# Kernel tuning notes

Hardware: AMD Instinct MI355X
Metric: run time of the kernel (lower is better)

The kernel has to match this reference:

```python
import jax, jax.numpy as jnp
import numpy as np

DIM = 2048
NUM_EXPERTS = 64
K = 2
TEMPERATURE = 1.0


def setup_inputs() -> dict:
    key = jax.random.key(0)
    kx, kw, kb = jax.random.split(key, 3)
    x = jax.random.normal(kx, (4, 4096, DIM), dtype=jnp.float32)
    # nn.Linear(dim, num_experts): weight [num_experts, dim], bias [num_experts]
    bound = 1.0 / np.sqrt(DIM)
    W = jax.random.uniform(kw, (NUM_EXPERTS, DIM), dtype=jnp.float32, minval=-bound, maxval=bound)
    b = jax.random.uniform(kb, (NUM_EXPERTS,), dtype=jnp.float32, minval=-bound, maxval=bound)
    return {"x": x, "W": W, "b": b}


def reference(x, W, b):
    # logits: (batch, seq, num_experts)
    logits = (jnp.einsum('bsd,ed->bse', x, W) + b) / TEMPERATURE
    probs = jax.nn.softmax(logits, axis=-1)
    values, indices = jax.lax.top_k(probs, K)
    return indices, values
```

## Files before the change

### kernel.cpp

```cpp
#include <hip/hip_runtime.h>
#include <math.h>

typedef _Float16 half8 __attribute__((ext_vector_type(8)));
typedef float f32x16 __attribute__((ext_vector_type(16)));

#define DIMK 2048
#define NEXP 64
#define BM 32
#define NW 4
#define KPW (DIMK / NW)
#define CHUNK 32
#define NCHUNK (KPW / CHUNK)
#define KSTEP 16
#define NKS (CHUNK / KSTEP)
#define NU (KPW / KSTEP)

__global__ void SwitchRouter_wsplit(const float* __restrict__ W, _Float16* __restrict__ ws) {
    int t = blockIdx.x * 256 + threadIdx.x;
    if (t >= NEXP * DIMK) return;
    int e = t >> 11, k = t & (DIMK - 1);
    float w = W[e * DIMK + k];
    _Float16 h0 = (_Float16)w;
    _Float16 h1 = (_Float16)(w - (float)h0);
    int kb8 = k >> 3, kj = k & 7;
    ws[(((kb8 * 2 + 0) << 9) + (e << 3) + kj)] = h0;
    ws[(((kb8 * 2 + 1) << 9) + (e << 3) + kj)] = h1;
}

__device__ __forceinline__ bool gt_pair(float v, int i, float v2, int i2) {
    return (v > v2) || (v == v2 && i < i2);
}

__device__ __forceinline__ half8 ldw(const _Float16* wsp, int kglob0, int half_, int et, int limb, int row) {
    int kb8 = (kglob0 >> 3) + half_;
    return *(const half8*)(wsp + (((size_t)(kb8 * 2 + limb) << 9) + (((et << 5) + row) << 3)));
}

__global__ __launch_bounds__(256, 3)
void SwitchRouter_43078521979510_kernel(const float* __restrict__ x,
                                        const _Float16* __restrict__ wsp,
                                        const float* __restrict__ bias,
                                        float* __restrict__ out, int M)
{
    __shared__ float lds[8704];

    const int t     = threadIdx.x;
    const int wv    = t >> 6;
    const int lane  = t & 63;
    const int row   = lane & 31;
    const int half_ = lane >> 5;
    const int r0    = blockIdx.x * BM;
    const int kwb   = wv * KPW;

    float* atile = lds + wv * 2048;
    const float* xg0 = x + (size_t)r0 * DIMK + kwb;

#define STAGE(c)                                                                   \
    {                                                                              \
        float* dst = atile + ((c) & 1) * 1024;                                     \
        _Pragma("unroll") for (int j = 0; j < 4; ++j) {                            \
            const int rowj = j * 8 + (lane >> 3);                                  \
            const float* src = xg0 + (size_t)rowj * DIMK + (c) * CHUNK             \
                               + (((lane & 7) ^ (rowj & 7)) << 2);                 \
            __builtin_amdgcn_global_load_lds(                                      \
                (const __attribute__((address_space(1))) void*)src,                \
                (__attribute__((address_space(3))) void*)(dst + j * 256),          \
                16, 0, 0);                                                         \
        }                                                                          \
    }

#define LOADW(u, slot)                                                             \
    {                                                                              \
        const int kg = kwb + (u) * KSTEP;                                          \
        wr[slot][0] = ldw(wsp, kg, half_, 0, 0, row);                              \
        wr[slot][1] = ldw(wsp, kg, half_, 0, 1, row);                              \
        wr[slot][2] = ldw(wsp, kg, half_, 1, 0, row);                              \
        wr[slot][3] = ldw(wsp, kg, half_, 1, 1, row);                              \
    }

    half8 wr[4][4];
    f32x16 acc[2] = {};

    LOADW(0, 0);
    LOADW(1, 1);
    LOADW(2, 2);
    STAGE(0);
    STAGE(1);

    for (int cb = 0; cb < NCHUNK / 2; ++cb) {
#pragma unroll
        for (int pc = 0; pc < 2; ++pc) {
            const int c = 2 * cb + pc;
            if (cb == NCHUNK / 2 - 1 && pc == 1) {
                asm volatile("s_waitcnt vmcnt(0)" ::: "memory");
            } else {
                asm volatile("s_waitcnt vmcnt(4)" ::: "memory");
            }

            const float* buf = atile + pc * 1024;

            float4 fA[NKS], fB[NKS];
#pragma unroll
            for (int ks = 0; ks < NKS; ++ks) {
                const int g  = ks * 4 + half_ * 2;
                const int s0 = g ^ (row & 7);
                const int s1 = (g + 1) ^ (row & 7);
                fA[ks] = *(const float4*)&buf[row * 32 + s0 * 4];
                fB[ks] = *(const float4*)&buf[row * 32 + s1 * 4];
            }
            asm volatile("s_waitcnt lgkmcnt(0)" ::: "memory");
            if (c + 2 < NCHUNK) STAGE(c + 2);

#pragma unroll
            for (int ks = 0; ks < NKS; ++ks) {
                const int u = c * NKS + ks;
                const int slot = (2 * pc + ks) & 3;
                if (u + 3 < NU) LOADW(u + 3, (slot + 3) & 3);

                const float4 va = fA[ks], vb = fB[ks];
                const float f[8] = {va.x, va.y, va.z, va.w, vb.x, vb.y, vb.z, vb.w};
                half8 a0, a1;
#pragma unroll
                for (int j = 0; j < 8; ++j) {
                    _Float16 h = (_Float16)f[j];
                    a0[j] = h;
                    a1[j] = (_Float16)(f[j] - (float)h);
                }

                const half8* w = wr[slot];
                acc[0] = __builtin_amdgcn_mfma_f32_32x32x16_f16(a0, w[0], acc[0], 0, 0, 0);
                acc[0] = __builtin_amdgcn_mfma_f32_32x32x16_f16(a1, w[0], acc[0], 0, 0, 0);
                acc[0] = __builtin_amdgcn_mfma_f32_32x32x16_f16(a0, w[1], acc[0], 0, 0, 0);
                acc[1] = __builtin_amdgcn_mfma_f32_32x32x16_f16(a0, w[2], acc[1], 0, 0, 0);
                acc[1] = __builtin_amdgcn_mfma_f32_32x32x16_f16(a1, w[2], acc[1], 0, 0, 0);
                acc[1] = __builtin_amdgcn_mfma_f32_32x32x16_f16(a0, w[3], acc[1], 0, 0, 0);
            }
        }
    }

    __syncthreads();
    float* red = lds;
#pragma unroll
    for (int s = 0; s < 16; ++s) {
        const int rowD = (s & 3) + 8 * (s >> 2) + 4 * half_;
        red[wv * 2176 + rowD * 68 + 0 * 32 + row] = acc[0][s];
        red[wv * 2176 + rowD * 68 + 1 * 32 + row] = acc[1][s];
    }
    __syncthreads();

    {
        const int rr = t >> 3;
        const int g8 = t & 7;
        float l[8];
#pragma unroll
        for (int j = 0; j < 8; ++j) {
            float s = 0.f;
#pragma unroll
            for (int w2 = 0; w2 < NW; ++w2) s += red[w2 * 2176 + rr * 68 + g8 * 8 + j];
            l[j] = s + bias[g8 * 8 + j];
        }

        float v0 = l[0];
        int   i0 = 8 * g8;
        float v1 = -INFINITY;
        int   i1 = -1;
#pragma unroll
        for (int j = 1; j < 8; ++j) {
            const float lv = l[j];
            const int   e  = 8 * g8 + j;
            if (lv > v0) { v1 = v0; i1 = i0; v0 = lv; i0 = e; }
            else if (lv > v1) { v1 = lv; i1 = e; }
        }
#pragma unroll
        for (int m2 = 1; m2 <= 4; m2 <<= 1) {
            const float ov0 = __shfl_xor(v0, m2);
            const int   oi0 = __shfl_xor(i0, m2);
            const float ov1 = __shfl_xor(v1, m2);
            const int   oi1 = __shfl_xor(i1, m2);
            if (gt_pair(ov0, oi0, v0, i0)) {
                if (gt_pair(v0, i0, ov1, oi1)) { v1 = v0; i1 = i0; }
                else                           { v1 = ov1; i1 = oi1; }
                v0 = ov0; i0 = oi0;
            } else if (gt_pair(ov0, oi0, v1, i1)) {
                v1 = ov0; i1 = oi0;
            }
        }
        float d = 0.f;
#pragma unroll
        for (int j = 0; j < 8; ++j) d += expf(l[j] - v0);
#pragma unroll
        for (int m2 = 1; m2 <= 4; m2 <<= 1) d += __shfl_xor(d, m2);

        if (g8 == 0) {
            const int R = r0 + rr;
            out[2 * R]     = (float)i0;
            out[2 * R + 1] = (float)i1;
            out[2 * M + 2 * R]     = 1.f / d;
            out[2 * M + 2 * R + 1] = expf(v1 - v0) / d;
        }
    }
}

extern "C" void kernel_launch(void* const* d_in, const int* in_sizes, int n_in,
                              void* d_out, int out_size, void* d_ws, size_t ws_size,
                              hipStream_t stream) {
    const float* x  = (const float*)d_in[0];
    const float* W  = (const float*)d_in[1];
    const float* b  = (const float*)d_in[2];
    float* out = (float*)d_out;
    _Float16* ws = (_Float16*)d_ws;
    const int M = in_sizes[0] / DIMK;

    SwitchRouter_wsplit<<<(NEXP * DIMK + 255) / 256, 256, 0, stream>>>(W, ws);
    SwitchRouter_43078521979510_kernel<<<M / BM, 256, 0, stream>>>(x, ws, b, out, M);
}
```

Measured before the change: 34.13 us.

## Fuse weight fp16 split into main kernel, drop separate preprocessing launch

Removes the separate kernel that split W into hi/lo fp16 limbs in a workspace. The main kernel now loads fp32 W directly through a two-slot register ring and does the hi/lo conversion inline before the MFMAs, with the vmcnt waits retuned to match. This cuts one kernel launch and the extra workspace write and read, at the cost of redundant per-block W conversion ALU work and double-width W loads.

```diff
diff --git a/kernel.cpp b/kernel.cpp
--- a/kernel.cpp
+++ b/kernel.cpp
@@ -13,32 +13,14 @@
 #define NCHUNK (KPW / CHUNK)
 #define KSTEP 16
 #define NKS (CHUNK / KSTEP)
-#define NU (KPW / KSTEP)
-
-__global__ void SwitchRouter_wsplit(const float* __restrict__ W, _Float16* __restrict__ ws) {
-    int t = blockIdx.x * 256 + threadIdx.x;
-    if (t >= NEXP * DIMK) return;
-    int e = t >> 11, k = t & (DIMK - 1);
-    float w = W[e * DIMK + k];
-    _Float16 h0 = (_Float16)w;
-    _Float16 h1 = (_Float16)(w - (float)h0);
-    int kb8 = k >> 3, kj = k & 7;
-    ws[(((kb8 * 2 + 0) << 9) + (e << 3) + kj)] = h0;
-    ws[(((kb8 * 2 + 1) << 9) + (e << 3) + kj)] = h1;
-}
 
 __device__ __forceinline__ bool gt_pair(float v, int i, float v2, int i2) {
     return (v > v2) || (v == v2 && i < i2);
 }
 
-__device__ __forceinline__ half8 ldw(const _Float16* wsp, int kglob0, int half_, int et, int limb, int row) {
-    int kb8 = (kglob0 >> 3) + half_;
-    return *(const half8*)(wsp + (((size_t)(kb8 * 2 + limb) << 9) + (((et << 5) + row) << 3)));
-}
-
 __global__ __launch_bounds__(256, 3)
 void SwitchRouter_43078521979510_kernel(const float* __restrict__ x,
-                                        const _Float16* __restrict__ wsp,
+                                        const float* __restrict__ W,
                                         const float* __restrict__ bias,
                                         float* __restrict__ out, int M)
 {
@@ -54,6 +36,7 @@
 
     float* atile = lds + wv * 2048;
     const float* xg0 = x + (size_t)r0 * DIMK + kwb;
+    const float* wbase0 = W + (size_t)row * DIMK + kwb + half_ * 8;
 
 #define STAGE(c)                                                                   \
     {                                                                              \
@@ -69,21 +52,54 @@
         }                                                                          \
     }
 
-#define LOADW(u, slot)                                                             \
-    {                                                                              \
-        const int kg = kwb + (u) * KSTEP;                                          \
-        wr[slot][0] = ldw(wsp, kg, half_, 0, 0, row);                              \
-        wr[slot][1] = ldw(wsp, kg, half_, 0, 1, row);                              \
-        wr[slot][2] = ldw(wsp, kg, half_, 1, 0, row);                              \
-        wr[slot][3] = ldw(wsp, kg, half_, 1, 1, row);                              \
-    }
-
-    half8 wr[4][4];
+#define LOADW2(c2, slot)                                                           \
+    {                                                                              \
+        _Pragma("unroll") for (int ks2 = 0; ks2 < 2; ++ks2)                        \
+        _Pragma("unroll") for (int et = 0; et < 2; ++et)                           \
+        _Pragma("unroll") for (int h = 0; h < 2; ++h)                              \
+            wring[slot][ks2][et][h] = *(const float4*)(wbase0                      \
+                + (size_t)et * 32 * DIMK + ((c2) * CHUNK + ks2 * KSTEP + h * 4));  \
+    }
+
+#define CONVW(slot, ks2)                                                           \
+    {                                                                              \
+        _Pragma("unroll") for (int et = 0; et < 2; ++et) {                         \
+            const float4 va = wring[slot][ks2][et][0], vb = wring[slot][ks2][et][1]; \
+            const float f[8] = {va.x, va.y, va.z, va.w, vb.x, vb.y, vb.z, vb.w};   \
+            _Pragma("unroll") for (int j = 0; j < 8; ++j) {                        \
+                _Float16 h = (_Float16)f[j];                                       \
+                w0[et][j] = h;                                                     \
+                w1[et][j] = (_Float16)(f[j] - (float)h);                           \
+            }                                                                      \
+        }                                                                          \
+    }
+
+#define DOMFMA()                                                                   \
+    {                                                                              \
+        acc[0] = __builtin_amdgcn_mfma_f32_32x32x16_f16(a0, w0[0], acc[0], 0, 0, 0); \
+        acc[0] = __builtin_amdgcn_mfma_f32_32x32x16_f16(a1, w0[0], acc[0], 0, 0, 0); \
+        acc[0] = __builtin_amdgcn_mfma_f32_32x32x16_f16(a0, w1[0], acc[0], 0, 0, 0); \
+        acc[1] = __builtin_amdgcn_mfma_f32_32x32x16_f16(a0, w0[1], acc[1], 0, 0, 0); \
+        acc[1] = __builtin_amdgcn_mfma_f32_32x32x16_f16(a1, w0[1], acc[1], 0, 0, 0); \
+        acc[1] = __builtin_amdgcn_mfma_f32_32x32x16_f16(a0, w1[1], acc[1], 0, 0, 0); \
+    }
+
+#define CONVA(ks2)                                                                 \
+    {                                                                              \
+        const float4 va = fA[ks2], vb = fB[ks2];                                   \
+        const float f[8] = {va.x, va.y, va.z, va.w, vb.x, vb.y, vb.z, vb.w};       \
+        _Pragma("unroll") for (int j = 0; j < 8; ++j) {                            \
+            _Float16 h = (_Float16)f[j];                                           \
+            a0[j] = h;                                                             \
+            a1[j] = (_Float16)(f[j] - (float)h);                                   \
+        }                                                                          \
+    }
+
+    float4 wring[2][2][2][2];
     f32x16 acc[2] = {};
 
-    LOADW(0, 0);
-    LOADW(1, 1);
-    LOADW(2, 2);
+    LOADW2(0, 0);
+    LOADW2(1, 1);
     STAGE(0);
     STAGE(1);
 
@@ -91,10 +107,12 @@
 #pragma unroll
         for (int pc = 0; pc < 2; ++pc) {
             const int c = 2 * cb + pc;
-            if (cb == NCHUNK / 2 - 1 && pc == 1) {
+            if (cb == 0 && pc == 0) {
+                asm volatile("s_waitcnt vmcnt(4)" ::: "memory");
+            } else if (cb == NCHUNK / 2 - 1 && pc == 1) {
                 asm volatile("s_waitcnt vmcnt(0)" ::: "memory");
             } else {
-                asm volatile("s_waitcnt vmcnt(4)" ::: "memory");
+                asm volatile("s_waitcnt vmcnt(12)" ::: "memory");
             }
 
             const float* buf = atile + pc * 1024;
@@ -108,33 +126,22 @@
                 fA[ks] = *(const float4*)&buf[row * 32 + s0 * 4];
                 fB[ks] = *(const float4*)&buf[row * 32 + s1 * 4];
             }
+
+            half8 w0[2], w1[2], a0, a1;
+
+            CONVW(pc, 0);
+
             asm volatile("s_waitcnt lgkmcnt(0)" ::: "memory");
             if (c + 2 < NCHUNK) STAGE(c + 2);
 
-#pragma unroll
-            for (int ks = 0; ks < NKS; ++ks) {
-                const int u = c * NKS + ks;
-                const int slot = (2 * pc + ks) & 3;
-                if (u + 3 < NU) LOADW(u + 3, (slot + 3) & 3);
-
-                const float4 va = fA[ks], vb = fB[ks];
-                const float f[8] = {va.x, va.y, va.z, va.w, vb.x, vb.y, vb.z, vb.w};
-                half8 a0, a1;
-#pragma unroll
-                for (int j = 0; j < 8; ++j) {
-                    _Float16 h = (_Float16)f[j];
-                    a0[j] = h;
-                    a1[j] = (_Float16)(f[j] - (float)h);
-                }
-
-                const half8* w = wr[slot];
-                acc[0] = __builtin_amdgcn_mfma_f32_32x32x16_f16(a0, w[0], acc[0], 0, 0, 0);
-                acc[0] = __builtin_amdgcn_mfma_f32_32x32x16_f16(a1, w[0], acc[0], 0, 0, 0);
-                acc[0] = __builtin_amdgcn_mfma_f32_32x32x16_f16(a0, w[1], acc[0], 0, 0, 0);
-                acc[1] = __builtin_amdgcn_mfma_f32_32x32x16_f16(a0, w[2], acc[1], 0, 0, 0);
-                acc[1] = __builtin_amdgcn_mfma_f32_32x32x16_f16(a1, w[2], acc[1], 0, 0, 0);
-                acc[1] = __builtin_amdgcn_mfma_f32_32x32x16_f16(a0, w[3], acc[1], 0, 0, 0);
-            }
+            CONVA(0);
+            DOMFMA();
+
+            CONVW(pc, 1);
+            if (c + 2 < NCHUNK) LOADW2(c + 2, pc);
+
+            CONVA(1);
+            DOMFMA();
         }
     }
 
@@ -208,9 +215,6 @@
     const float* W  = (const float*)d_in[1];
     const float* b  = (const float*)d_in[2];
     float* out = (float*)d_out;
-    _Float16* ws = (_Float16*)d_ws;
     const int M = in_sizes[0] / DIMK;
-
-    SwitchRouter_wsplit<<<(NEXP * DIMK + 255) / 256, 256, 0, stream>>>(W, ws);
-    SwitchRouter_43078521979510_kernel<<<M / BM, 256, 0, stream>>>(x, ws, b, out, M);
+    SwitchRouter_43078521979510_kernel<<<M / BM, 256, 0, stream>>>(x, W, b, out, M);
 }
```

Result: slower. 44.18 us (+29.4%).

## Split K across eight waves with explicit pipeline and tree reduction

Applied to the files above, without the earlier changes.

Doubles the waves per block from 4 to 8, so each wave covers a 256-wide K slice. The chunk loop is unrolled by hand into an explicit software pipeline with tuned vmcnt waits and a two-slot weight register buffer. The cross-wave partial sum becomes a staged tree reduction through LDS, replacing the single all-wave store. The aim is more latency hiding and more concurrent loads per block, at the cost of extra barriers and a larger LDS footprint (64KB) that may limit occupancy.

```diff
diff --git a/kernel.cpp b/kernel.cpp
--- a/kernel.cpp
+++ b/kernel.cpp
@@ -7,13 +7,11 @@
 #define DIMK 2048
 #define NEXP 64
 #define BM 32
-#define NW 4
+#define NW 8
 #define KPW (DIMK / NW)
 #define CHUNK 32
 #define NCHUNK (KPW / CHUNK)
 #define KSTEP 16
-#define NKS (CHUNK / KSTEP)
-#define NU (KPW / KSTEP)
 
 __global__ void SwitchRouter_wsplit(const float* __restrict__ W, _Float16* __restrict__ ws) {
     int t = blockIdx.x * 256 + threadIdx.x;
@@ -36,13 +34,13 @@
     return *(const half8*)(wsp + (((size_t)(kb8 * 2 + limb) << 9) + (((et << 5) + row) << 3)));
 }
 
-__global__ __launch_bounds__(256, 3)
+__global__ __launch_bounds__(512, 4)
 void SwitchRouter_43078521979510_kernel(const float* __restrict__ x,
                                         const _Float16* __restrict__ wsp,
                                         const float* __restrict__ bias,
                                         float* __restrict__ out, int M)
 {
-    __shared__ float lds[8704];
+    __shared__ float lds[16384];
 
     const int t     = threadIdx.x;
     const int wv    = t >> 6;
@@ -78,87 +76,133 @@
         wr[slot][3] = ldw(wsp, kg, half_, 1, 1, row);                              \
     }
 
-    half8 wr[4][4];
+#define DSRD(pc)                                                                   \
+    {                                                                              \
+        const float* buf = atile + (pc) * 1024;                                    \
+        _Pragma("unroll") for (int ks = 0; ks < 2; ++ks) {                         \
+            const int g = ks * 4 + half_ * 2;                                      \
+            fA[ks] = *(const float4*)&buf[row * 32 + ((g ^ (row & 7)) << 2)];      \
+            fB[ks] = *(const float4*)&buf[row * 32 + (((g + 1) ^ (row & 7)) << 2)];\
+        }                                                                          \
+        asm volatile("s_waitcnt lgkmcnt(0)" ::: "memory");                         \
+    }
+
+#define KS(ks, slot)                                                               \
+    {                                                                              \
+        const float4 va = fA[ks], vb = fB[ks];                                     \
+        const float f[8] = {va.x, va.y, va.z, va.w, vb.x, vb.y, vb.z, vb.w};       \
+        half8 a0, a1;                                                              \
+        _Pragma("unroll") for (int j = 0; j < 8; ++j) {                            \
+            _Float16 h = (_Float16)f[j];                                           \
+            a0[j] = h;                                                             \
+            a1[j] = (_Float16)(f[j] - (float)h);                                   \
+        }                                                                          \
+        acc[0] = __builtin_amdgcn_mfma_f32_32x32x16_f16(a0, wr[slot][0], acc[0], 0, 0, 0); \
+        acc[0] = __builtin_amdgcn_mfma_f32_32x32x16_f16(a1, wr[slot][0], acc[0], 0, 0, 0); \
+        acc[0] = __builtin_amdgcn_mfma_f32_32x32x16_f16(a0, wr[slot][1], acc[0], 0, 0, 0); \
+        acc[1] = __builtin_amdgcn_mfma_f32_32x32x16_f16(a0, wr[slot][2], acc[1], 0, 0, 0); \
+        acc[1] = __builtin_amdgcn_mfma_f32_32x32x16_f16(a1, wr[slot][2], acc[1], 0, 0, 0); \
+        acc[1] = __builtin_amdgcn_mfma_f32_32x32x16_f16(a0, wr[slot][3], acc[1], 0, 0, 0); \
+    }
+
+    half8 wr[2][4];
+    float4 fA[2], fB[2];
     f32x16 acc[2] = {};
 
-    LOADW(0, 0);
-    LOADW(1, 1);
-    LOADW(2, 2);
-    STAGE(0);
-    STAGE(1);
-
-    for (int cb = 0; cb < NCHUNK / 2; ++cb) {
-#pragma unroll
-        for (int pc = 0; pc < 2; ++pc) {
-            const int c = 2 * cb + pc;
-            if (cb == NCHUNK / 2 - 1 && pc == 1) {
-                asm volatile("s_waitcnt vmcnt(0)" ::: "memory");
-            } else {
-                asm volatile("s_waitcnt vmcnt(4)" ::: "memory");
+    LOADW(0, 0); LOADW(1, 1);
+    STAGE(0); STAGE(1);
+
+    asm volatile("s_waitcnt vmcnt(4)" ::: "memory");
+    DSRD(0);
+    STAGE(2);
+    KS(0, 0); LOADW(2, 0);
+    KS(1, 1); LOADW(3, 1);
+
+    asm volatile("s_waitcnt vmcnt(12)" ::: "memory");
+    DSRD(1);
+    STAGE(3);
+    asm volatile("s_waitcnt vmcnt(8)" ::: "memory");
+    KS(0, 0); LOADW(4, 0);
+    asm volatile("s_waitcnt vmcnt(8)" ::: "memory");
+    KS(1, 1); LOADW(5, 1);
+
+    for (int cb = 1; cb <= 2; ++cb) {
+        const int c0 = 2 * cb;
+        DSRD(0);
+        STAGE(c0 + 2);
+        asm volatile("s_waitcnt vmcnt(8)" ::: "memory");
+        KS(0, 0); LOADW(2 * c0 + 2, 0);
+        asm volatile("s_waitcnt vmcnt(8)" ::: "memory");
+        KS(1, 1); LOADW(2 * c0 + 3, 1);
+        DSRD(1);
+        STAGE(c0 + 3);
+        asm volatile("s_waitcnt vmcnt(8)" ::: "memory");
+        KS(0, 0); LOADW(2 * c0 + 4, 0);
+        asm volatile("s_waitcnt vmcnt(8)" ::: "memory");
+        KS(1, 1); LOADW(2 * c0 + 5, 1);
+    }
+
+    DSRD(0);
+    asm volatile("s_waitcnt vmcnt(4)" ::: "memory");
+    KS(0, 0); LOADW(14, 0);
+    asm volatile("s_waitcnt vmcnt(4)" ::: "memory");
+    KS(1, 1); LOADW(15, 1);
+
+    DSRD(1);
+    asm volatile("s_waitcnt vmcnt(4)" ::: "memory");
+    KS(0, 0);
+    asm volatile("s_waitcnt vmcnt(0)" ::: "memory");
+    KS(1, 1);
+
+    __syncthreads();
+    float* red = lds;
+
+#define TILE_STORE(slot)                                                           \
+    {                                                                              \
+        _Pragma("unroll") for (int et = 0; et < 2; ++et)                           \
+        _Pragma("unroll") for (int s = 0; s < 16; ++s) {                           \
+            const int rowD = (s & 3) + 8 * (s >> 2) + 4 * half_;                   \
+            red[(slot) * 2176 + rowD * 68 + et * 32 + row] = acc[et][s];           \
+        }                                                                          \
+    }
+#define TILE_ADD(slot)                                                             \
+    {                                                                              \
+        _Pragma("unroll") for (int et = 0; et < 2; ++et)                           \
+        _Pragma("unroll") for (int s = 0; s < 16; ++s) {                           \
+            const int rowD = (s & 3) + 8 * (s >> 2) + 4 * half_;                   \
+            acc[et][s] += red[(slot) * 2176 + rowD * 68 + et * 32 + row];          \
+        }                                                                          \
+    }
+
+    if (wv & 1) TILE_STORE(wv >> 1);
+    __syncthreads();
+    if (!(wv & 1)) TILE_ADD(wv >> 1);
+    __syncthreads();
+    if (wv == 2 || wv == 6) TILE_STORE(wv >> 2);
+    __syncthreads();
+    if (wv == 0 || wv == 4) TILE_ADD(wv >> 2);
+    __syncthreads();
+    if (wv == 4) TILE_STORE(0);
+    __syncthreads();
+    if (wv == 0) {
+        TILE_ADD(0);
+#pragma unroll
+        for (int et = 0; et < 2; ++et)
+#pragma unroll
+            for (int s = 0; s < 16; ++s) {
+                const int rowD = (s & 3) + 8 * (s >> 2) + 4 * half_;
+                red[rowD * 68 + et * 32 + row] = acc[et][s];
             }
-
-            const float* buf = atile + pc * 1024;
-
-            float4 fA[NKS], fB[NKS];
-#pragma unroll
-            for (int ks = 0; ks < NKS; ++ks) {
-                const int g  = ks * 4 + half_ * 2;
-                const int s0 = g ^ (row & 7);
-                const int s1 = (g + 1) ^ (row & 7);
-                fA[ks] = *(const float4*)&buf[row * 32 + s0 * 4];
-                fB[ks] = *(const float4*)&buf[row * 32 + s1 * 4];
-            }
-            asm volatile("s_waitcnt lgkmcnt(0)" ::: "memory");
-            if (c + 2 < NCHUNK) STAGE(c + 2);
-
-#pragma unroll
-            for (int ks = 0; ks < NKS; ++ks) {
-                const int u = c * NKS + ks;
-                const int slot = (2 * pc + ks) & 3;
-                if (u + 3 < NU) LOADW(u + 3, (slot + 3) & 3);
-
-                const float4 va = fA[ks], vb = fB[ks];
-                const float f[8] = {va.x, va.y, va.z, va.w, vb.x, vb.y, vb.z, vb.w};
-                half8 a0, a1;
-#pragma unroll
-                for (int j = 0; j < 8; ++j) {
-                    _Float16 h = (_Float16)f[j];
-                    a0[j] = h;
-                    a1[j] = (_Float16)(f[j] - (float)h);
-                }
-
-                const half8* w = wr[slot];
-                acc[0] = __builtin_amdgcn_mfma_f32_32x32x16_f16(a0, w[0], acc[0], 0, 0, 0);
-                acc[0] = __builtin_amdgcn_mfma_f32_32x32x16_f16(a1, w[0], acc[0], 0, 0, 0);
-                acc[0] = __builtin_amdgcn_mfma_f32_32x32x16_f16(a0, w[1], acc[0], 0, 0, 0);
-                acc[1] = __builtin_amdgcn_mfma_f32_32x32x16_f16(a0, w[2], acc[1], 0, 0, 0);
-                acc[1] = __builtin_amdgcn_mfma_f32_32x32x16_f16(a1, w[2], acc[1], 0, 0, 0);
-                acc[1] = __builtin_amdgcn_mfma_f32_32x32x16_f16(a0, w[3], acc[1], 0, 0, 0);
-            }
-        }
-    }
-
-    __syncthreads();
-    float* red = lds;
-#pragma unroll
-    for (int s = 0; s < 16; ++s) {
-        const int rowD = (s & 3) + 8 * (s >> 2) + 4 * half_;
-        red[wv * 2176 + rowD * 68 + 0 * 32 + row] = acc[0][s];
-        red[wv * 2176 + rowD * 68 + 1 * 32 + row] = acc[1][s];
-    }
-    __syncthreads();
-
-    {
+    }
+    __syncthreads();
+
+    if (t < BM * 8) {
         const int rr = t >> 3;
         const int g8 = t & 7;
         float l[8];
 #pragma unroll
-        for (int j = 0; j < 8; ++j) {
-            float s = 0.f;
-#pragma unroll
-            for (int w2 = 0; w2 < NW; ++w2) s += red[w2 * 2176 + rr * 68 + g8 * 8 + j];
-            l[j] = s + bias[g8 * 8 + j];
-        }
+        for (int j = 0; j < 8; ++j)
+            l[j] = red[rr * 68 + g8 * 8 + j] + bias[g8 * 8 + j];
 
         float v0 = l[0];
         int   i0 = 8 * g8;
@@ -212,5 +256,5 @@
     const int M = in_sizes[0] / DIMK;
 
     SwitchRouter_wsplit<<<(NEXP * DIMK + 255) / 256, 256, 0, stream>>>(W, ws);
-    SwitchRouter_43078521979510_kernel<<<M / BM, 256, 0, stream>>>(x, ws, b, out, M);
-}
+    SwitchRouter_43078521979510_kernel<<<M / BM, 512, 0, stream>>>(x, ws, b, out, M);
+}
```

Result: slower. 40.65 us (+19.1%).
